# Performance work log

Hardware: AMD Instinct MI355X
Metric: run time of the kernel (lower is better)

Reference implementation:

```python
import jax, jax.numpy as jnp
import numpy as np

N, E, B = 100000, 1200000, 512
IN_DIM, HID, K, NCLS = 64, 64, 3, 10


def setup_inputs() -> dict:
    key = jax.random.key(0)
    ks = jax.random.split(key, 10)
    features = jax.random.normal(ks[0], (N, IN_DIM), jnp.float32)
    edge_src = jax.random.randint(ks[1], (E,), 0, N)
    edge_dst = jax.random.randint(ks[2], (E,), 0, N)
    graph_ids = jnp.sort(jax.random.randint(ks[3], (N,), 0, B))
    s1 = float(1.0 / np.sqrt(IN_DIM))
    W1 = jax.random.uniform(ks[4], (IN_DIM, HID), jnp.float32, -s1, s1)
    b1 = jnp.zeros((HID,), jnp.float32)
    s2 = float(1.0 / np.sqrt(HID))
    W2 = jax.random.uniform(ks[5], (HID, HID), jnp.float32, -s2, s2)
    b2 = jnp.zeros((HID,), jnp.float32)
    s3 = float(1.0 / np.sqrt(HID * 3))
    cw = jax.random.uniform(ks[6], (HID, HID, 3), jnp.float32, -s3, s3)
    cb = jax.random.uniform(ks[7], (HID,), jnp.float32, -s3, s3)
    Wc = jax.random.uniform(ks[8], (HID, NCLS), jnp.float32, -s2, s2)
    bc = jax.random.uniform(ks[9], (NCLS,), jnp.float32, -s2, s2)
    return dict(features=features, edge_src=edge_src, edge_dst=edge_dst,
                graph_ids=graph_ids, num_graphs=B,
                W1=W1, b1=b1, W2=W2, b2=b2, cw=cw, cb=cb, Wc=Wc, bc=bc)


def graph_conv(h, src, dst, W, b, n_nodes):
    # DGL GraphConv, norm='both', allow_zero_in_degree (degrees clamped to 1)
    ones = jnp.ones((src.shape[0],), h.dtype)
    out_deg = jnp.zeros((n_nodes,), h.dtype).at[src].add(ones)
    in_deg = jnp.zeros((n_nodes,), h.dtype).at[dst].add(ones)
    norm_s = jax.lax.rsqrt(jnp.clip(out_deg, 1.0, None))
    norm_d = jax.lax.rsqrt(jnp.clip(in_deg, 1.0, None))
    m = (h * norm_s[:, None]) @ W  # weight first; math identical to agg-first
    agg = jnp.zeros((n_nodes, W.shape[1]), h.dtype).at[dst].add(m[src])
    return agg * norm_d[:, None] + b


def sort_pool(h, gid, num_graphs, k):
    # DGL SortPooling: sort each node's features ascending along feature dim,
    # then take top-k nodes per graph by last feature value (descending),
    # zero-padding graphs with < k nodes. Output [num_graphs, k*D].
    hs = jnp.sort(h, axis=-1)
    key = hs[:, -1]
    order = jnp.lexsort((-key, gid))  # gid asc, key desc
    gid_s = gid[order]
    hs_s = hs[order]
    n = gid.shape[0]
    start = jnp.full((num_graphs,), n).at[gid_s].min(jnp.arange(n))
    rank = jnp.arange(n) - start[gid_s]  # within-graph rank by key desc
    mask = rank < k
    slot = gid_s * k + jnp.clip(rank, 0, k - 1)
    out = jnp.zeros((num_graphs * k, hs.shape[-1]), h.dtype).at[slot].add(
        jnp.where(mask[:, None], hs_s, jnp.zeros((), h.dtype)))
    return out.reshape(num_graphs, k * hs.shape[-1])


def reference(features, edge_src, edge_dst, graph_ids, num_graphs,
              W1, b1, W2, b2, cw, cb, Wc, bc):
    n = features.shape[0]
    h = jax.nn.relu(graph_conv(features, edge_src, edge_dst, W1, b1, n))
    h = jax.nn.relu(graph_conv(h, edge_src, edge_dst, W2, b2, n))
    p = sort_pool(h, graph_ids, num_graphs, K)          # [B, K*HID]
    x = p.reshape(num_graphs, HID, K)                    # faithful torch reshape
    # Conv1d(kernel=3, stride=1) on length-3 input -> length-1 output
    y = jax.nn.relu(jnp.einsum('bct,oct->bo', x, cw) + cb)
    return y @ Wc + bc
```

## Files before the change

### kernel.cpp

```cpp
#include <hip/hip_runtime.h>
#include <hip/hip_bf16.h>


#define PART_H 50176
#define QPART_H (PART_H / 4)
#define PART_F 25088
#define QUART_F (PART_F / 4)
#define MCH  64

__global__ void __launch_bounds__(256) k_histgemm(
    const int* __restrict__ esrc, const int* __restrict__ edst,
    unsigned char* __restrict__ hd, unsigned char* __restrict__ hs,
    const float* __restrict__ in, const float* __restrict__ W,
    float* __restrict__ mout, int N, int E, int PH, int histBlocks) {
  __shared__ float smem[12800];
  const int t = threadIdx.x;
  if (blockIdx.x < histBlocks) {
    unsigned int* lc = (unsigned int*)smem;
    const int b = blockIdx.x;
    const int half = PH * MCH;
    const int a = b / half;
    const int r = b % half;
    const int p = r % PH;
    const int m = r / PH;
    const int* __restrict__ arr = a ? esrc : edst;
    unsigned char* __restrict__ outp = a ? hs : hd;
    const int base = p * PART_H;
    const int lim = min(PART_H, N - base);
    for (int i = t; i < QPART_H; i += 256) lc[i] = 0u;
    __syncthreads();
    const long long cb = (long long)m * E / MCH;
    const long long ce = (long long)(m + 1) * E / MCH;
    const long long a0 = min((cb + 3) & ~3LL, ce);
    const long long nv = (ce - a0) >> 2;
    for (long long e = cb + t; e < a0; e += 256) {
      int d = arr[e] - base;
      if ((unsigned)d < (unsigned)lim) atomicAdd(&lc[d >> 2], 1u << ((d & 3) * 8));
    }
    const int4* __restrict__ a4p = (const int4*)(arr + a0);
    for (long long i = t; i < nv; i += 256) {
      int4 v4 = a4p[i];
      int d;
      d = v4.x - base; if ((unsigned)d < (unsigned)lim) atomicAdd(&lc[d >> 2], 1u << ((d & 3) * 8));
      d = v4.y - base; if ((unsigned)d < (unsigned)lim) atomicAdd(&lc[d >> 2], 1u << ((d & 3) * 8));
      d = v4.z - base; if ((unsigned)d < (unsigned)lim) atomicAdd(&lc[d >> 2], 1u << ((d & 3) * 8));
      d = v4.w - base; if ((unsigned)d < (unsigned)lim) atomicAdd(&lc[d >> 2], 1u << ((d & 3) * 8));
    }
    for (long long e = a0 + (nv << 2) + t; e < ce; e += 256) {
      int d = arr[e] - base;
      if ((unsigned)d < (unsigned)lim) atomicAdd(&lc[d >> 2], 1u << ((d & 3) * 8));
    }
    __syncthreads();
    unsigned char* slice = outp + ((size_t)p * MCH + m) * PART_H;
    for (int i = t; i < lim; i += 256)
      slice[i] = (unsigned char)((lc[i >> 2] >> ((i & 3) * 8)) & 0xffu);
  } else {
    float* Wl = smem;
    float* Ac = smem + 4096;
    const int ch = (t & 7) * 8;
    const int nb = (t >> 3) * 4;
    for (int i = t; i < 1024; i += 256)
      ((float4*)Wl)[i] = ((const float4*)W)[i];
    const int gb = blockIdx.x - histBlocks;
    const int ng = gridDim.x - histBlocks;
    const int NT = (N + 127) >> 7;
    for (int tile = gb; tile < NT; tile += ng) {
      const int vbase = tile << 7;
      __syncthreads();
      for (int i = t; i < 2048; i += 256) {
        const int r = i >> 4;
        const int c = (i & 15) * 4;
        const int v = vbase + r;
        float4 val = make_float4(0.f, 0.f, 0.f, 0.f);
        if (v < N) val = *(const float4*)(in + (size_t)v * 64 + c);
        Ac[(c + 0) * 136 + r] = val.x;
        Ac[(c + 1) * 136 + r] = val.y;
        Ac[(c + 2) * 136 + r] = val.z;
        Ac[(c + 3) * 136 + r] = val.w;
      }
      __syncthreads();
      float acc[4][8];
#pragma unroll
      for (int j = 0; j < 4; ++j)
#pragma unroll
        for (int c = 0; c < 8; ++c) acc[j][c] = 0.f;
      for (int k = 0; k < 64; k += 4) {
#pragma unroll
        for (int kk = 0; kk < 4; ++kk) {
          const float4 aa = *(const float4*)&Ac[(k + kk) * 136 + nb];
          const float4 w0 = *(const float4*)&Wl[(k + kk) * 64 + ch];
          const float4 w1 = *(const float4*)&Wl[(k + kk) * 64 + ch + 4];
          const float an[4] = {aa.x, aa.y, aa.z, aa.w};
          const float wn[8] = {w0.x, w0.y, w0.z, w0.w, w1.x, w1.y, w1.z, w1.w};
#pragma unroll
          for (int j = 0; j < 4; ++j)
#pragma unroll
            for (int c = 0; c < 8; ++c)
              acc[j][c] = fmaf(an[j], wn[c], acc[j][c]);
        }
      }
#pragma unroll
      for (int j = 0; j < 4; ++j) {
        const int v = vbase + nb + j;
        if (v < N) {
          float4 o0, o1;
          o0.x = acc[j][0]; o0.y = acc[j][1]; o0.z = acc[j][2]; o0.w = acc[j][3];
          o1.x = acc[j][4]; o1.y = acc[j][5]; o1.z = acc[j][6]; o1.w = acc[j][7];
          *(float4*)(mout + (size_t)v * 64 + ch)     = o0;
          *(float4*)(mout + (size_t)v * 64 + ch + 4) = o1;
        }
      }
    }
  }
}

__global__ void k_off(unsigned char* __restrict__ hd, const unsigned char* __restrict__ hs,
                      int* __restrict__ deg_d, float* __restrict__ norm_s,
                      float* __restrict__ norm_d, int* __restrict__ gstart,
                      int B, int N) {
  int v = blockIdx.x * blockDim.x + threadIdx.x;
  if (v >= N) return;
  if (v < B) gstart[v] = 0x7f7f7f7f;
  size_t base = (size_t)(v / PART_H) * MCH * PART_H + (v % PART_H);
  int run = 0;
#pragma unroll
  for (int m = 0; m < MCH; ++m) {
    int t = hd[base + (size_t)m * PART_H];
    hd[base + (size_t)m * PART_H] = (unsigned char)run;
    run += t;
  }
  int s = 0;
#pragma unroll
  for (int m = 0; m < MCH; ++m) s += hs[base + (size_t)m * PART_H];
  deg_d[v] = run;
  norm_d[v] = rsqrtf((float)max(run, 1));
  norm_s[v] = rsqrtf((float)max(s, 1));
}

__global__ void k_scan1(const int* __restrict__ deg, int* __restrict__ rowptr,
                        int* __restrict__ bsum, int N) {
  __shared__ int sums[256];
  const int t = threadIdx.x;
  const int base = blockIdx.x * 2048 + t * 8;
  int loc[8];
  int tot = 0;
#pragma unroll
  for (int j = 0; j < 8; ++j) {
    int idx = base + j;
    loc[j] = tot;
    tot += (idx < N) ? deg[idx] : 0;
  }
  sums[t] = tot;
  __syncthreads();
  for (int off = 1; off < 256; off <<= 1) {
    int x = (t >= off) ? sums[t - off] : 0;
    __syncthreads();
    sums[t] += x;
    __syncthreads();
  }
  int excl = (t == 0) ? 0 : sums[t - 1];
#pragma unroll
  for (int j = 0; j < 8; ++j) {
    int idx = base + j;
    if (idx < N) rowptr[idx] = excl + loc[j];
  }
  if (t == 255) bsum[blockIdx.x] = sums[255];
}

__global__ void k_scan2(int* __restrict__ bsum, int nb) {
  int lane = threadIdx.x;
  int v = (lane < nb) ? bsum[lane] : 0;
  int inc = v;
#pragma unroll
  for (int off = 1; off < 64; off <<= 1) {
    int o = __shfl_up(inc, off, 64);
    if (lane >= off) inc += o;
  }
  if (lane < nb) bsum[lane] = inc - v;
}

__global__ void k_fill2(const int* __restrict__ esrc, const int* __restrict__ edst,
                        const unsigned char* __restrict__ hd, const int* __restrict__ rowptr,
                        const int* __restrict__ bsum, int* __restrict__ csr,
                        int N, int E, int PF) {
  __shared__ unsigned int cur4[QUART_F];
  const int b = blockIdx.x;
  const int p = b % PF;
  const int m = b / PF;
  const int base = p * PART_F;
  const int lim = min(PART_F, N - base);
  const unsigned char* slice = hd + ((size_t)(p >> 1) * MCH + m) * PART_H
                                  + (size_t)(p & 1) * PART_F;
  const unsigned int* slice4 = (const unsigned int*)slice;
  for (int i = threadIdx.x; i < QUART_F; i += blockDim.x) cur4[i] = slice4[i];
  __syncthreads();
  const int* __restrict__ rp = rowptr + base;
  const long long cb = (long long)m * E / MCH;
  const long long ce = (long long)(m + 1) * E / MCH;
  const long long a0 = min((cb + 3) & ~3LL, ce);
  const long long nv = (ce - a0) >> 2;
  for (long long e = cb + threadIdx.x; e < a0; e += blockDim.x) {
    int d = edst[e] - base;
    if ((unsigned)d < (unsigned)lim) {
      unsigned int old = atomicAdd(&cur4[d >> 2], 1u << ((d & 3) * 8));
      csr[rp[d] + bsum[(base + d) >> 11] + ((old >> ((d & 3) * 8)) & 0xff)] = esrc[e];
    }
  }
  const int4* __restrict__ d4p = (const int4*)(edst + a0);
  const int4* __restrict__ s4p = (const int4*)(esrc + a0);
  for (long long i = threadIdx.x; i < nv; i += blockDim.x) {
    int4 d4 = d4p[i];
    int4 s4 = s4p[i];
    int d;
    d = d4.x - base;
    if ((unsigned)d < (unsigned)lim) {
      unsigned int old = atomicAdd(&cur4[d >> 2], 1u << ((d & 3) * 8));
      csr[rp[d] + bsum[(base + d) >> 11] + ((old >> ((d & 3) * 8)) & 0xff)] = s4.x;
    }
    d = d4.y - base;
    if ((unsigned)d < (unsigned)lim) {
      unsigned int old = atomicAdd(&cur4[d >> 2], 1u << ((d & 3) * 8));
      csr[rp[d] + bsum[(base + d) >> 11] + ((old >> ((d & 3) * 8)) & 0xff)] = s4.y;
    }
    d = d4.z - base;
    if ((unsigned)d < (unsigned)lim) {
      unsigned int old = atomicAdd(&cur4[d >> 2], 1u << ((d & 3) * 8));
      csr[rp[d] + bsum[(base + d) >> 11] + ((old >> ((d & 3) * 8)) & 0xff)] = s4.z;
    }
    d = d4.w - base;
    if ((unsigned)d < (unsigned)lim) {
      unsigned int old = atomicAdd(&cur4[d >> 2], 1u << ((d & 3) * 8));
      csr[rp[d] + bsum[(base + d) >> 11] + ((old >> ((d & 3) * 8)) & 0xff)] = s4.w;
    }
  }
  for (long long e = a0 + (nv << 2) + threadIdx.x; e < ce; e += blockDim.x) {
    int d = edst[e] - base;
    if ((unsigned)d < (unsigned)lim) {
      unsigned int old = atomicAdd(&cur4[d >> 2], 1u << ((d & 3) * 8));
      csr[rp[d] + bsum[(base + d) >> 11] + ((old >> ((d & 3) * 8)) & 0xff)] = esrc[e];
    }
  }
}

__global__ void __launch_bounds__(256) k_gemm64(
    const float* __restrict__ in, const float* __restrict__ norm,
    const float* __restrict__ W, float* __restrict__ out, int N) {
  __shared__ float Wl[4096];
  __shared__ float Ac[64 * 136];
  const int t = threadIdx.x;
  const int ch = (t & 7) * 8;
  const int nb = (t >> 3) * 4;
  for (int i = t; i < 1024; i += 256)
    ((float4*)Wl)[i] = ((const float4*)W)[i];
  const int NT = (N + 127) >> 7;
  for (int tile = blockIdx.x; tile < NT; tile += gridDim.x) {
    const int vbase = tile << 7;
    __syncthreads();
    for (int i = t; i < 2048; i += 256) {
      const int r = i >> 4;
      const int c = (i & 15) * 4;
      const int v = vbase + r;
      float4 val = make_float4(0.f, 0.f, 0.f, 0.f);
      if (v < N) val = *(const float4*)(in + (size_t)v * 64 + c);
      Ac[(c + 0) * 136 + r] = val.x;
      Ac[(c + 1) * 136 + r] = val.y;
      Ac[(c + 2) * 136 + r] = val.z;
      Ac[(c + 3) * 136 + r] = val.w;
    }
    __syncthreads();
    float acc[4][8];
#pragma unroll
    for (int j = 0; j < 4; ++j)
#pragma unroll
      for (int c = 0; c < 8; ++c) acc[j][c] = 0.f;
    for (int k = 0; k < 64; k += 4) {
#pragma unroll
      for (int kk = 0; kk < 4; ++kk) {
        const float4 aa = *(const float4*)&Ac[(k + kk) * 136 + nb];
        const float4 w0 = *(const float4*)&Wl[(k + kk) * 64 + ch];
        const float4 w1 = *(const float4*)&Wl[(k + kk) * 64 + ch + 4];
        const float an[4] = {aa.x, aa.y, aa.z, aa.w};
        const float wn[8] = {w0.x, w0.y, w0.z, w0.w, w1.x, w1.y, w1.z, w1.w};
#pragma unroll
        for (int j = 0; j < 4; ++j)
#pragma unroll
          for (int c = 0; c < 8; ++c)
            acc[j][c] = fmaf(an[j], wn[c], acc[j][c]);
      }
    }
#pragma unroll
    for (int j = 0; j < 4; ++j) {
      const int v = vbase + nb + j;
      if (v < N) {
        const float nm = norm[v];
        float4 o0, o1;
        o0.x = acc[j][0] * nm; o0.y = acc[j][1] * nm;
        o0.z = acc[j][2] * nm; o0.w = acc[j][3] * nm;
        o1.x = acc[j][4] * nm; o1.y = acc[j][5] * nm;
        o1.z = acc[j][6] * nm; o1.w = acc[j][7] * nm;
        *(float4*)(out + (size_t)v * 64 + ch)     = o0;
        *(float4*)(out + (size_t)v * 64 + ch + 4) = o1;
      }
    }
  }
}

__global__ void k_gather(const float* __restrict__ m, const int* __restrict__ rowptr,
                         const int* __restrict__ bsum,
                         const int* __restrict__ deg, const float* __restrict__ norm_d,
                         const float* __restrict__ bias, const int* __restrict__ csr,
                         const float* __restrict__ nsrc,
                         const int* __restrict__ gid, int* __restrict__ gstart,
                         float* __restrict__ h, float* __restrict__ key, int N) {
  const int w = blockIdx.x * (blockDim.x >> 6) + (threadIdx.x >> 6);
  if (w >= N) return;
  const int lane = threadIdx.x & 63;
  const int chb = (lane & 7) * 8;
  const int grp = lane >> 3;
  if (gid != nullptr && lane == 0) {
    int g = gid[w];
    if (w == 0 || gid[w - 1] != g) gstart[g] = w;
  }
  const int start = rowptr[w] + bsum[w >> 11];
  const int cnt = deg[w];
  float4 a00 = make_float4(0.f, 0.f, 0.f, 0.f);
  float4 a01 = make_float4(0.f, 0.f, 0.f, 0.f);
  float4 a10 = make_float4(0.f, 0.f, 0.f, 0.f);
  float4 a11 = make_float4(0.f, 0.f, 0.f, 0.f);
  int i = grp;
  if (nsrc != nullptr) {
    for (; i + 8 < cnt; i += 16) {
      int s0 = csr[start + i];
      int s1 = csr[start + i + 8];
      float n0 = nsrc[s0], n1 = nsrc[s1];
      const float* r0 = m + (size_t)s0 * 64 + chb;
      const float* r1 = m + (size_t)s1 * 64 + chb;
      const float4 v00 = *(const float4*)r0;
      const float4 v01 = *(const float4*)(r0 + 4);
      const float4 v10 = *(const float4*)r1;
      const float4 v11 = *(const float4*)(r1 + 4);
      a00.x = fmaf(v00.x, n0, a00.x); a00.y = fmaf(v00.y, n0, a00.y);
      a00.z = fmaf(v00.z, n0, a00.z); a00.w = fmaf(v00.w, n0, a00.w);
      a01.x = fmaf(v01.x, n0, a01.x); a01.y = fmaf(v01.y, n0, a01.y);
      a01.z = fmaf(v01.z, n0, a01.z); a01.w = fmaf(v01.w, n0, a01.w);
      a10.x = fmaf(v10.x, n1, a10.x); a10.y = fmaf(v10.y, n1, a10.y);
      a10.z = fmaf(v10.z, n1, a10.z); a10.w = fmaf(v10.w, n1, a10.w);
      a11.x = fmaf(v11.x, n1, a11.x); a11.y = fmaf(v11.y, n1, a11.y);
      a11.z = fmaf(v11.z, n1, a11.z); a11.w = fmaf(v11.w, n1, a11.w);
    }
    if (i < cnt) {
      int s0 = csr[start + i];
      float n0 = nsrc[s0];
      const float* r0 = m + (size_t)s0 * 64 + chb;
      const float4 v00 = *(const float4*)r0;
      const float4 v01 = *(const float4*)(r0 + 4);
      a00.x = fmaf(v00.x, n0, a00.x); a00.y = fmaf(v00.y, n0, a00.y);
      a00.z = fmaf(v00.z, n0, a00.z); a00.w = fmaf(v00.w, n0, a00.w);
      a01.x = fmaf(v01.x, n0, a01.x); a01.y = fmaf(v01.y, n0, a01.y);
      a01.z = fmaf(v01.z, n0, a01.z); a01.w = fmaf(v01.w, n0, a01.w);
    }
  } else {
    for (; i + 8 < cnt; i += 16) {
      int s0 = csr[start + i];
      int s1 = csr[start + i + 8];
      const float* r0 = m + (size_t)s0 * 64 + chb;
      const float* r1 = m + (size_t)s1 * 64 + chb;
      const float4 v00 = *(const float4*)r0;
      const float4 v01 = *(const float4*)(r0 + 4);
      const float4 v10 = *(const float4*)r1;
      const float4 v11 = *(const float4*)(r1 + 4);
      a00.x += v00.x; a00.y += v00.y; a00.z += v00.z; a00.w += v00.w;
      a01.x += v01.x; a01.y += v01.y; a01.z += v01.z; a01.w += v01.w;
      a10.x += v10.x; a10.y += v10.y; a10.z += v10.z; a10.w += v10.w;
      a11.x += v11.x; a11.y += v11.y; a11.z += v11.z; a11.w += v11.w;
    }
    if (i < cnt) {
      int s0 = csr[start + i];
      const float* r0 = m + (size_t)s0 * 64 + chb;
      const float4 v00 = *(const float4*)r0;
      const float4 v01 = *(const float4*)(r0 + 4);
      a00.x += v00.x; a00.y += v00.y; a00.z += v00.z; a00.w += v00.w;
      a01.x += v01.x; a01.y += v01.y; a01.z += v01.z; a01.w += v01.w;
    }
  }
  a00.x += a10.x; a00.y += a10.y; a00.z += a10.z; a00.w += a10.w;
  a01.x += a11.x; a01.y += a11.y; a01.z += a11.z; a01.w += a11.w;
#pragma unroll
  for (int off = 8; off <= 32; off <<= 1) {
    a00.x += __shfl_xor(a00.x, off, 64);
    a00.y += __shfl_xor(a00.y, off, 64);
    a00.z += __shfl_xor(a00.z, off, 64);
    a00.w += __shfl_xor(a00.w, off, 64);
    a01.x += __shfl_xor(a01.x, off, 64);
    a01.y += __shfl_xor(a01.y, off, 64);
    a01.z += __shfl_xor(a01.z, off, 64);
    a01.w += __shfl_xor(a01.w, off, 64);
  }
  const float nd = norm_d[w];
  const float4 b0 = *(const float4*)(bias + chb);
  const float4 b1 = *(const float4*)(bias + chb + 4);
  float4 o0, o1;
  o0.x = fmaxf(fmaf(a00.x, nd, b0.x), 0.f);
  o0.y = fmaxf(fmaf(a00.y, nd, b0.y), 0.f);
  o0.z = fmaxf(fmaf(a00.z, nd, b0.z), 0.f);
  o0.w = fmaxf(fmaf(a00.w, nd, b0.w), 0.f);
  o1.x = fmaxf(fmaf(a01.x, nd, b1.x), 0.f);
  o1.y = fmaxf(fmaf(a01.y, nd, b1.y), 0.f);
  o1.z = fmaxf(fmaf(a01.z, nd, b1.z), 0.f);
  o1.w = fmaxf(fmaf(a01.w, nd, b1.w), 0.f);
  if (grp == 0) {
    *(float4*)(h + (size_t)w * 64 + chb)     = o0;
    *(float4*)(h + (size_t)w * 64 + chb + 4) = o1;
  }
  if (key != nullptr) {
    float mx = fmaxf(fmaxf(fmaxf(o0.x, o0.y), fmaxf(o0.z, o0.w)),
                     fmaxf(fmaxf(o1.x, o1.y), fmaxf(o1.z, o1.w)));
#pragma unroll
    for (int off = 1; off < 8; off <<= 1) mx = fmaxf(mx, __shfl_xor(mx, off, 64));
    if (lane == 0) key[w] = mx;
  }
}

__global__ void __launch_bounds__(256) k_tail(
    const float* __restrict__ key, const int* __restrict__ gstart,
    const float* __restrict__ h,
    const float* __restrict__ cw, const float* __restrict__ cb,
    const float* __restrict__ Wc, const float* __restrict__ bc,
    float* __restrict__ out, int B, int N) {
  __shared__ int sel[3];
  __shared__ float prow[192];
  const int b = blockIdx.x;
  const int wid = threadIdx.x >> 6;
  const int lane = threadIdx.x & 63;

  if (wid == 0) {
    const int gs = gstart[b];
    int g2 = b + 1;
    while (g2 < B && gstart[g2] >= N) ++g2;
    const int ns = (g2 < B) ? gstart[g2] : N;
    const int s = gs;
    const int c = (gs < N) ? (ns - gs) : 0;
    float v0 = -1.f, v1 = -1.f, v2 = -1.f;
    int i0 = 0x7fffffff, i1 = 0x7fffffff, i2 = 0x7fffffff;
    for (int i = s + lane; i < s + c; i += 64) {
      float kv = key[i];
      if (kv > v0 || (kv == v0 && i < i0)) {
        v2 = v1; i2 = i1; v1 = v0; i1 = i0; v0 = kv; i0 = i;
      } else if (kv > v1 || (kv == v1 && i < i1)) {
        v2 = v1; i2 = i1; v1 = kv; i1 = i;
      } else if (kv > v2 || (kv == v2 && i < i2)) {
        v2 = kv; i2 = i;
      }
    }
    int ptr = 0;
    for (int r = 0; r < 3; ++r) {
      float mv = (ptr == 0) ? v0 : (ptr == 1) ? v1 : (ptr == 2) ? v2 : -1.f;
      int   mi = (ptr == 0) ? i0 : (ptr == 1) ? i1 : (ptr == 2) ? i2 : 0x7fffffff;
      float bv = mv; int bi = mi;
#pragma unroll
      for (int off = 32; off; off >>= 1) {
        float ov = __shfl_xor(bv, off, 64);
        int   oi = __shfl_xor(bi, off, 64);
        if (ov > bv || (ov == bv && oi < bi)) { bv = ov; bi = oi; }
      }
      if (bi == mi && ptr < 3) ptr++;
      if (lane == 0) sel[r] = (bi == 0x7fffffff) ? -1 : bi;
    }
  }
  __syncthreads();
  if (wid < 3) {
    int node = sel[wid];
    float v = 0.f;
    if (node >= 0) {
      v = h[(size_t)node * 64 + lane];
      for (int k2 = 2; k2 <= 64; k2 <<= 1) {
        for (int j = k2 >> 1; j > 0; j >>= 1) {
          float o = __shfl_xor(v, j, 64);
          bool up = ((lane & k2) == 0);
          bool lower = ((lane & j) == 0);
          v = (lower == up) ? fminf(v, o) : fmaxf(v, o);
        }
      }
    }
    prow[wid * 64 + lane] = v;
  }
  __syncthreads();
  if (wid == 0) {
    float y = cb[lane];
    for (int j = 0; j < 192; ++j) y = fmaf(prow[j], cw[lane * 192 + j], y);
    float ry = fmaxf(y, 0.f);
    for (int c = 0; c < 10; ++c) {
      float s = ry * Wc[lane * 10 + c];
#pragma unroll
      for (int off = 32; off; off >>= 1) s += __shfl_xor(s, off, 64);
      if (lane == 0) out[b * 10 + c] = s + bc[c];
    }
  }
}

extern "C" void kernel_launch(void* const* d_in, const int* in_sizes, int n_in,
                              void* d_out, int out_size, void* d_ws, size_t ws_size,
                              hipStream_t stream) {
  const float* features = (const float*)d_in[0];
  const int*   esrc     = (const int*)d_in[1];
  const int*   edst     = (const int*)d_in[2];
  const int*   gid      = (const int*)d_in[3];
  const float* W1 = (const float*)d_in[5];
  const float* b1 = (const float*)d_in[6];
  const float* W2 = (const float*)d_in[7];
  const float* b2 = (const float*)d_in[8];
  const float* cw = (const float*)d_in[9];
  const float* cb = (const float*)d_in[10];
  const float* Wc = (const float*)d_in[11];
  const float* bc = (const float*)d_in[12];
  float* out = (float*)d_out;

  const int N = in_sizes[0] / 64;
  const int E = in_sizes[1];
  const int B = out_size / 10;
  const size_t N64 = (size_t)N * 64;
  const int nscan = (N + 2047) / 2048;
  const int PH = (N + PART_H - 1) / PART_H;
  const int PF = (N + PART_F - 1) / PART_F;
  const size_t HSZ = (size_t)PH * MCH * PART_H;
  const int NT = (N + 127) / 128;
  const int histBlocks = 2 * PH * MCH;

  float* bufA   = (float*)d_ws;
  float* bufB   = bufA + N64;
  int*   deg_d  = (int*)(bufB + N64);
  float* norm_s = (float*)(deg_d + N);
  float* norm_d = norm_s + N;
  float* key    = norm_d + N;
  int*   rowptr = (int*)(key + N);
  int*   csr    = rowptr + N;
  int*   bsum   = csr + E;
  int*   gstart = bsum + 64;
  unsigned char* hd = (unsigned char*)(gstart + B);
  unsigned char* hs = hd + HSZ;

  const int TB = 256;

  k_histgemm<<<histBlocks + NT, TB, 0, stream>>>(esrc, edst, hd, hs,
                                                 features, W1, bufA,
                                                 N, E, PH, histBlocks);
  k_off<<<(N + TB - 1) / TB, TB, 0, stream>>>(hd, hs, deg_d, norm_s, norm_d,
                                              gstart, B, N);
  k_scan1<<<nscan, 256, 0, stream>>>(deg_d, rowptr, bsum, N);
  k_scan2<<<1, 64, 0, stream>>>(bsum, nscan);
  k_fill2<<<PF * MCH, TB, 0, stream>>>(esrc, edst, hd, rowptr, bsum, csr, N, E, PF);

  k_gather<<<(N + 3) / 4, TB, 0, stream>>>(bufA, rowptr, bsum, deg_d, norm_d, b1,
                                           csr, norm_s, nullptr, nullptr,
                                           bufB, nullptr, N);

  k_gemm64<<<NT, TB, 0, stream>>>(bufB, norm_s, W2, bufA, N);
  k_gather<<<(N + 3) / 4, TB, 0, stream>>>(bufA, rowptr, bsum, deg_d, norm_d, b2,
                                           csr, nullptr, gid, gstart,
                                           bufB, key, N);

  k_tail<<<B, TB, 0, stream>>>(key, gstart, bufB, cw, cb, Wc, bc, out, B, N);
}
```

Measured before the change: 301.1 us.

## Fuse degree offset pass into scan and make gather grid-stride

Merges the per-node histogram offset kernel with the first scan stage, so each thread reads its 8 nodes' per-chunk byte counts as one 64-bit word and computes degrees, norms, and the local prefix sum in a single launch. The hd buffer is aligned to 16 bytes so these 64-bit accesses are valid. The two gather launches become a fixed grid of 2048 blocks with a grid-stride loop over nodes, and the bias load is hoisted out of the loop. This saves one launch and the deg_d round trip. The packed byte counts assume per-chunk degrees fit in 8 bits with no carry across lanes, and the fixed gather grid may balance load differently across nodes.

```diff
diff --git a/kernel.cpp b/kernel.cpp
--- a/kernel.cpp
+++ b/kernel.cpp
@@ -114,41 +114,45 @@
   }
 }
 
-__global__ void k_off(unsigned char* __restrict__ hd, const unsigned char* __restrict__ hs,
-                      int* __restrict__ deg_d, float* __restrict__ norm_s,
-                      float* __restrict__ norm_d, int* __restrict__ gstart,
-                      int B, int N) {
-  int v = blockIdx.x * blockDim.x + threadIdx.x;
-  if (v >= N) return;
-  if (v < B) gstart[v] = 0x7f7f7f7f;
-  size_t base = (size_t)(v / PART_H) * MCH * PART_H + (v % PART_H);
-  int run = 0;
-#pragma unroll
-  for (int m = 0; m < MCH; ++m) {
-    int t = hd[base + (size_t)m * PART_H];
-    hd[base + (size_t)m * PART_H] = (unsigned char)run;
-    run += t;
-  }
-  int s = 0;
-#pragma unroll
-  for (int m = 0; m < MCH; ++m) s += hs[base + (size_t)m * PART_H];
-  deg_d[v] = run;
-  norm_d[v] = rsqrtf((float)max(run, 1));
-  norm_s[v] = rsqrtf((float)max(s, 1));
-}
-
-__global__ void k_scan1(const int* __restrict__ deg, int* __restrict__ rowptr,
-                        int* __restrict__ bsum, int N) {
+__global__ void __launch_bounds__(256) k_offscan(
+    unsigned char* __restrict__ hd, const unsigned char* __restrict__ hs,
+    int* __restrict__ deg_d, float* __restrict__ norm_s, float* __restrict__ norm_d,
+    int* __restrict__ gstart, int* __restrict__ rowptr, int* __restrict__ bsum,
+    int B, int N) {
   __shared__ int sums[256];
   const int t = threadIdx.x;
-  const int base = blockIdx.x * 2048 + t * 8;
+  const int v0 = blockIdx.x * 2048 + t * 8;
+#pragma unroll
+  for (int j = 0; j < 8; ++j)
+    if (v0 + j < B) gstart[v0 + j] = 0x7f7f7f7f;
+  unsigned long long drun = 0ull, stot = 0ull;
+  if (v0 < N) {
+    const size_t rb = (size_t)(v0 / PART_H) * MCH * PART_H + (size_t)(v0 % PART_H);
+    unsigned long long* __restrict__ hd8 = (unsigned long long*)(hd + rb);
+    const unsigned long long* __restrict__ hs8 = (const unsigned long long*)(hs + rb);
+    const size_t st8 = PART_H / 8;
+#pragma unroll 8
+    for (int m = 0; m < MCH; ++m) {
+      unsigned long long c = hd8[(size_t)m * st8];
+      hd8[(size_t)m * st8] = drun;
+      drun += c;
+      stot += hs8[(size_t)m * st8];
+    }
+  }
   int loc[8];
   int tot = 0;
 #pragma unroll
   for (int j = 0; j < 8; ++j) {
-    int idx = base + j;
+    const int v = v0 + j;
+    const int dg = (v < N) ? (int)((drun >> (8 * j)) & 0xffull) : 0;
     loc[j] = tot;
-    tot += (idx < N) ? deg[idx] : 0;
+    tot += dg;
+    if (v < N) {
+      deg_d[v] = dg;
+      norm_d[v] = rsqrtf((float)max(dg, 1));
+      const int so = (int)((stot >> (8 * j)) & 0xffull);
+      norm_s[v] = rsqrtf((float)max(so, 1));
+    }
   }
   sums[t] = tot;
   __syncthreads();
@@ -161,8 +165,8 @@
   int excl = (t == 0) ? 0 : sums[t - 1];
 #pragma unroll
   for (int j = 0; j < 8; ++j) {
-    int idx = base + j;
-    if (idx < N) rowptr[idx] = excl + loc[j];
+    const int v = v0 + j;
+    if (v < N) rowptr[v] = excl + loc[j];
   }
   if (t == 255) bsum[blockIdx.x] = sums[255];
 }
@@ -312,112 +316,114 @@
                          const float* __restrict__ nsrc,
                          const int* __restrict__ gid, int* __restrict__ gstart,
                          float* __restrict__ h, float* __restrict__ key, int N) {
-  const int w = blockIdx.x * (blockDim.x >> 6) + (threadIdx.x >> 6);
-  if (w >= N) return;
+  const int wpb = blockDim.x >> 6;
+  const int nwaves = gridDim.x * wpb;
   const int lane = threadIdx.x & 63;
   const int chb = (lane & 7) * 8;
   const int grp = lane >> 3;
-  if (gid != nullptr && lane == 0) {
-    int g = gid[w];
-    if (w == 0 || gid[w - 1] != g) gstart[g] = w;
-  }
-  const int start = rowptr[w] + bsum[w >> 11];
-  const int cnt = deg[w];
-  float4 a00 = make_float4(0.f, 0.f, 0.f, 0.f);
-  float4 a01 = make_float4(0.f, 0.f, 0.f, 0.f);
-  float4 a10 = make_float4(0.f, 0.f, 0.f, 0.f);
-  float4 a11 = make_float4(0.f, 0.f, 0.f, 0.f);
-  int i = grp;
-  if (nsrc != nullptr) {
-    for (; i + 8 < cnt; i += 16) {
-      int s0 = csr[start + i];
-      int s1 = csr[start + i + 8];
-      float n0 = nsrc[s0], n1 = nsrc[s1];
-      const float* r0 = m + (size_t)s0 * 64 + chb;
-      const float* r1 = m + (size_t)s1 * 64 + chb;
-      const float4 v00 = *(const float4*)r0;
-      const float4 v01 = *(const float4*)(r0 + 4);
-      const float4 v10 = *(const float4*)r1;
-      const float4 v11 = *(const float4*)(r1 + 4);
-      a00.x = fmaf(v00.x, n0, a00.x); a00.y = fmaf(v00.y, n0, a00.y);
-      a00.z = fmaf(v00.z, n0, a00.z); a00.w = fmaf(v00.w, n0, a00.w);
-      a01.x = fmaf(v01.x, n0, a01.x); a01.y = fmaf(v01.y, n0, a01.y);
-      a01.z = fmaf(v01.z, n0, a01.z); a01.w = fmaf(v01.w, n0, a01.w);
-      a10.x = fmaf(v10.x, n1, a10.x); a10.y = fmaf(v10.y, n1, a10.y);
-      a10.z = fmaf(v10.z, n1, a10.z); a10.w = fmaf(v10.w, n1, a10.w);
-      a11.x = fmaf(v11.x, n1, a11.x); a11.y = fmaf(v11.y, n1, a11.y);
-      a11.z = fmaf(v11.z, n1, a11.z); a11.w = fmaf(v11.w, n1, a11.w);
-    }
-    if (i < cnt) {
-      int s0 = csr[start + i];
-      float n0 = nsrc[s0];
-      const float* r0 = m + (size_t)s0 * 64 + chb;
-      const float4 v00 = *(const float4*)r0;
-      const float4 v01 = *(const float4*)(r0 + 4);
-      a00.x = fmaf(v00.x, n0, a00.x); a00.y = fmaf(v00.y, n0, a00.y);
-      a00.z = fmaf(v00.z, n0, a00.z); a00.w = fmaf(v00.w, n0, a00.w);
-      a01.x = fmaf(v01.x, n0, a01.x); a01.y = fmaf(v01.y, n0, a01.y);
-      a01.z = fmaf(v01.z, n0, a01.z); a01.w = fmaf(v01.w, n0, a01.w);
-    }
-  } else {
-    for (; i + 8 < cnt; i += 16) {
-      int s0 = csr[start + i];
-      int s1 = csr[start + i + 8];
-      const float* r0 = m + (size_t)s0 * 64 + chb;
-      const float* r1 = m + (size_t)s1 * 64 + chb;
-      const float4 v00 = *(const float4*)r0;
-      const float4 v01 = *(const float4*)(r0 + 4);
-      const float4 v10 = *(const float4*)r1;
-      const float4 v11 = *(const float4*)(r1 + 4);
-      a00.x += v00.x; a00.y += v00.y; a00.z += v00.z; a00.w += v00.w;
-      a01.x += v01.x; a01.y += v01.y; a01.z += v01.z; a01.w += v01.w;
-      a10.x += v10.x; a10.y += v10.y; a10.z += v10.z; a10.w += v10.w;
-      a11.x += v11.x; a11.y += v11.y; a11.z += v11.z; a11.w += v11.w;
-    }
-    if (i < cnt) {
-      int s0 = csr[start + i];
-      const float* r0 = m + (size_t)s0 * 64 + chb;
-      const float4 v00 = *(const float4*)r0;
-      const float4 v01 = *(const float4*)(r0 + 4);
-      a00.x += v00.x; a00.y += v00.y; a00.z += v00.z; a00.w += v00.w;
-      a01.x += v01.x; a01.y += v01.y; a01.z += v01.z; a01.w += v01.w;
-    }
-  }
-  a00.x += a10.x; a00.y += a10.y; a00.z += a10.z; a00.w += a10.w;
-  a01.x += a11.x; a01.y += a11.y; a01.z += a11.z; a01.w += a11.w;
-#pragma unroll
-  for (int off = 8; off <= 32; off <<= 1) {
-    a00.x += __shfl_xor(a00.x, off, 64);
-    a00.y += __shfl_xor(a00.y, off, 64);
-    a00.z += __shfl_xor(a00.z, off, 64);
-    a00.w += __shfl_xor(a00.w, off, 64);
-    a01.x += __shfl_xor(a01.x, off, 64);
-    a01.y += __shfl_xor(a01.y, off, 64);
-    a01.z += __shfl_xor(a01.z, off, 64);
-    a01.w += __shfl_xor(a01.w, off, 64);
-  }
-  const float nd = norm_d[w];
   const float4 b0 = *(const float4*)(bias + chb);
   const float4 b1 = *(const float4*)(bias + chb + 4);
-  float4 o0, o1;
-  o0.x = fmaxf(fmaf(a00.x, nd, b0.x), 0.f);
-  o0.y = fmaxf(fmaf(a00.y, nd, b0.y), 0.f);
-  o0.z = fmaxf(fmaf(a00.z, nd, b0.z), 0.f);
-  o0.w = fmaxf(fmaf(a00.w, nd, b0.w), 0.f);
-  o1.x = fmaxf(fmaf(a01.x, nd, b1.x), 0.f);
-  o1.y = fmaxf(fmaf(a01.y, nd, b1.y), 0.f);
-  o1.z = fmaxf(fmaf(a01.z, nd, b1.z), 0.f);
-  o1.w = fmaxf(fmaf(a01.w, nd, b1.w), 0.f);
-  if (grp == 0) {
-    *(float4*)(h + (size_t)w * 64 + chb)     = o0;
-    *(float4*)(h + (size_t)w * 64 + chb + 4) = o1;
-  }
-  if (key != nullptr) {
-    float mx = fmaxf(fmaxf(fmaxf(o0.x, o0.y), fmaxf(o0.z, o0.w)),
-                     fmaxf(fmaxf(o1.x, o1.y), fmaxf(o1.z, o1.w)));
-#pragma unroll
-    for (int off = 1; off < 8; off <<= 1) mx = fmaxf(mx, __shfl_xor(mx, off, 64));
-    if (lane == 0) key[w] = mx;
+  for (int w = blockIdx.x * wpb + (threadIdx.x >> 6); w < N; w += nwaves) {
+    if (gid != nullptr && lane == 0) {
+      int g = gid[w];
+      if (w == 0 || gid[w - 1] != g) gstart[g] = w;
+    }
+    const int start = rowptr[w] + bsum[w >> 11];
+    const int cnt = deg[w];
+    float4 a00 = make_float4(0.f, 0.f, 0.f, 0.f);
+    float4 a01 = make_float4(0.f, 0.f, 0.f, 0.f);
+    float4 a10 = make_float4(0.f, 0.f, 0.f, 0.f);
+    float4 a11 = make_float4(0.f, 0.f, 0.f, 0.f);
+    int i = grp;
+    if (nsrc != nullptr) {
+      for (; i + 8 < cnt; i += 16) {
+        int s0 = csr[start + i];
+        int s1 = csr[start + i + 8];
+        float n0 = nsrc[s0], n1 = nsrc[s1];
+        const float* r0 = m + (size_t)s0 * 64 + chb;
+        const float* r1 = m + (size_t)s1 * 64 + chb;
+        const float4 v00 = *(const float4*)r0;
+        const float4 v01 = *(const float4*)(r0 + 4);
+        const float4 v10 = *(const float4*)r1;
+        const float4 v11 = *(const float4*)(r1 + 4);
+        a00.x = fmaf(v00.x, n0, a00.x); a00.y = fmaf(v00.y, n0, a00.y);
+        a00.z = fmaf(v00.z, n0, a00.z); a00.w = fmaf(v00.w, n0, a00.w);
+        a01.x = fmaf(v01.x, n0, a01.x); a01.y = fmaf(v01.y, n0, a01.y);
+        a01.z = fmaf(v01.z, n0, a01.z); a01.w = fmaf(v01.w, n0, a01.w);
+        a10.x = fmaf(v10.x, n1, a10.x); a10.y = fmaf(v10.y, n1, a10.y);
+        a10.z = fmaf(v10.z, n1, a10.z); a10.w = fmaf(v10.w, n1, a10.w);
+        a11.x = fmaf(v11.x, n1, a11.x); a11.y = fmaf(v11.y, n1, a11.y);
+        a11.z = fmaf(v11.z, n1, a11.z); a11.w = fmaf(v11.w, n1, a11.w);
+      }
+      if (i < cnt) {
+        int s0 = csr[start + i];
+        float n0 = nsrc[s0];
+        const float* r0 = m + (size_t)s0 * 64 + chb;
+        const float4 v00 = *(const float4*)r0;
+        const float4 v01 = *(const float4*)(r0 + 4);
+        a00.x = fmaf(v00.x, n0, a00.x); a00.y = fmaf(v00.y, n0, a00.y);
+        a00.z = fmaf(v00.z, n0, a00.z); a00.w = fmaf(v00.w, n0, a00.w);
+        a01.x = fmaf(v01.x, n0, a01.x); a01.y = fmaf(v01.y, n0, a01.y);
+        a01.z = fmaf(v01.z, n0, a01.z); a01.w = fmaf(v01.w, n0, a01.w);
+      }
+    } else {
+      for (; i + 8 < cnt; i += 16) {
+        int s0 = csr[start + i];
+        int s1 = csr[start + i + 8];
+        const float* r0 = m + (size_t)s0 * 64 + chb;
+        const float* r1 = m + (size_t)s1 * 64 + chb;
+        const float4 v00 = *(const float4*)r0;
+        const float4 v01 = *(const float4*)(r0 + 4);
+        const float4 v10 = *(const float4*)r1;
+        const float4 v11 = *(const float4*)(r1 + 4);
+        a00.x += v00.x; a00.y += v00.y; a00.z += v00.z; a00.w += v00.w;
+        a01.x += v01.x; a01.y += v01.y; a01.z += v01.z; a01.w += v01.w;
+        a10.x += v10.x; a10.y += v10.y; a10.z += v10.z; a10.w += v10.w;
+        a11.x += v11.x; a11.y += v11.y; a11.z += v11.z; a11.w += v11.w;
+      }
+      if (i < cnt) {
+        int s0 = csr[start + i];
+        const float* r0 = m + (size_t)s0 * 64 + chb;
+        const float4 v00 = *(const float4*)r0;
+        const float4 v01 = *(const float4*)(r0 + 4);
+        a00.x += v00.x; a00.y += v00.y; a00.z += v00.z; a00.w += v00.w;
+        a01.x += v01.x; a01.y += v01.y; a01.z += v01.z; a01.w += v01.w;
+      }
+    }
+    a00.x += a10.x; a00.y += a10.y; a00.z += a10.z; a00.w += a10.w;
+    a01.x += a11.x; a01.y += a11.y; a01.z += a11.z; a01.w += a11.w;
+#pragma unroll
+    for (int off = 8; off <= 32; off <<= 1) {
+      a00.x += __shfl_xor(a00.x, off, 64);
+      a00.y += __shfl_xor(a00.y, off, 64);
+      a00.z += __shfl_xor(a00.z, off, 64);
+      a00.w += __shfl_xor(a00.w, off, 64);
+      a01.x += __shfl_xor(a01.x, off, 64);
+      a01.y += __shfl_xor(a01.y, off, 64);
+      a01.z += __shfl_xor(a01.z, off, 64);
+      a01.w += __shfl_xor(a01.w, off, 64);
+    }
+    const float nd = norm_d[w];
+    float4 o0, o1;
+    o0.x = fmaxf(fmaf(a00.x, nd, b0.x), 0.f);
+    o0.y = fmaxf(fmaf(a00.y, nd, b0.y), 0.f);
+    o0.z = fmaxf(fmaf(a00.z, nd, b0.z), 0.f);
+    o0.w = fmaxf(fmaf(a00.w, nd, b0.w), 0.f);
+    o1.x = fmaxf(fmaf(a01.x, nd, b1.x), 0.f);
+    o1.y = fmaxf(fmaf(a01.y, nd, b1.y), 0.f);
+    o1.z = fmaxf(fmaf(a01.z, nd, b1.z), 0.f);
+    o1.w = fmaxf(fmaf(a01.w, nd, b1.w), 0.f);
+    if (grp == 0) {
+      *(float4*)(h + (size_t)w * 64 + chb)     = o0;
+      *(float4*)(h + (size_t)w * 64 + chb + 4) = o1;
+    }
+    if (key != nullptr) {
+      float mx = fmaxf(fmaxf(fmaxf(o0.x, o0.y), fmaxf(o0.z, o0.w)),
+                       fmaxf(fmaxf(o1.x, o1.y), fmaxf(o1.z, o1.w)));
+#pragma unroll
+      for (int off = 1; off < 8; off <<= 1) mx = fmaxf(mx, __shfl_xor(mx, off, 64));
+      if (lane == 0) key[w] = mx;
+    }
   }
 }
 
@@ -536,7 +542,7 @@
   int*   csr    = rowptr + N;
   int*   bsum   = csr + E;
   int*   gstart = bsum + 64;
-  unsigned char* hd = (unsigned char*)(gstart + B);
+  unsigned char* hd = (unsigned char*)(((size_t)(gstart + B) + 15) & ~(size_t)15);
   unsigned char* hs = hd + HSZ;
 
   const int TB = 256;
@@ -544,20 +550,21 @@
   k_histgemm<<<histBlocks + NT, TB, 0, stream>>>(esrc, edst, hd, hs,
                                                  features, W1, bufA,
                                                  N, E, PH, histBlocks);
-  k_off<<<(N + TB - 1) / TB, TB, 0, stream>>>(hd, hs, deg_d, norm_s, norm_d,
-                                              gstart, B, N);
-  k_scan1<<<nscan, 256, 0, stream>>>(deg_d, rowptr, bsum, N);
+  k_offscan<<<nscan, 256, 0, stream>>>(hd, hs, deg_d, norm_s, norm_d,
+                                       gstart, rowptr, bsum, B, N);
   k_scan2<<<1, 64, 0, stream>>>(bsum, nscan);
   k_fill2<<<PF * MCH, TB, 0, stream>>>(esrc, edst, hd, rowptr, bsum, csr, N, E, PF);
 
-  k_gather<<<(N + 3) / 4, TB, 0, stream>>>(bufA, rowptr, bsum, deg_d, norm_d, b1,
-                                           csr, norm_s, nullptr, nullptr,
-                                           bufB, nullptr, N);
+  const int GB = 2048;
+
+  k_gather<<<GB, TB, 0, stream>>>(bufA, rowptr, bsum, deg_d, norm_d, b1,
+                                  csr, norm_s, nullptr, nullptr,
+                                  bufB, nullptr, N);
 
   k_gemm64<<<NT, TB, 0, stream>>>(bufB, norm_s, W2, bufA, N);
-  k_gather<<<(N + 3) / 4, TB, 0, stream>>>(bufA, rowptr, bsum, deg_d, norm_d, b2,
-                                           csr, nullptr, gid, gstart,
-                                           bufB, key, N);
+  k_gather<<<GB, TB, 0, stream>>>(bufA, rowptr, bsum, deg_d, norm_d, b2,
+                                  csr, nullptr, gid, gstart,
+                                  bufB, key, N);
 
   k_tail<<<B, TB, 0, stream>>>(key, gstart, bufB, cw, cb, Wc, bc, out, B, N);
 }
```

New measurement: 329.5 us. 1.09x slower.
